# Kernel tuning notes

Hardware: AMD Instinct MI355X
Metric: run time of the kernel (lower is better)

The kernel has to match this reference:

```python
import jax, jax.numpy as jnp
import numpy as np

D = 2048      # hidden
H = 16        # heads
HD = 128      # head dim
E = 64        # experts
K = 8         # top-k
F = 1024      # expert intermediate
B, S = 1, 256
EPS = 1e-05
THETA = 10000.0
SCALE = 0.08838834764831845  # 1/sqrt(128)


def _rms(x, w):
    return x * jax.lax.rsqrt(jnp.mean(x * x, axis=-1, keepdims=True) + EPS) * w


def _rotate_half(x):
    h = x.shape[-1] // 2
    return jnp.concatenate([-x[..., h:], x[..., :h]], axis=-1)


def setup_inputs() -> dict:
    key = jax.random.key(0)
    ks = jax.random.split(key, 16)
    std = 0.02
    return {
        "x": jax.random.normal(ks[0], (B, S, D), jnp.float32),
        "ln1_w": jnp.ones((D,), jnp.float32),
        "q_w": jax.random.normal(ks[1], (D, D), jnp.float32) * std,
        "k_w": jax.random.normal(ks[2], (D, D), jnp.float32) * std,
        "v_w": jax.random.normal(ks[3], (D, D), jnp.float32) * std,
        "o_w": jax.random.normal(ks[4], (D, D), jnp.float32) * std,
        "qn_w": jnp.ones((D,), jnp.float32),
        "kn_w": jnp.ones((D,), jnp.float32),
        "ln2_w": jnp.ones((D,), jnp.float32),
        "router_w": jax.random.normal(ks[5], (E, D), jnp.float32) * std,
        "gate_w": jax.random.normal(ks[6], (E, F, D), jnp.float32) * std,
        "up_w": jax.random.normal(ks[7], (E, F, D), jnp.float32) * std,
        "down_w": jax.random.normal(ks[8], (E, D, F), jnp.float32) * std,
    }


def reference(x, ln1_w, q_w, k_w, v_w, o_w, qn_w, kn_w, ln2_w,
              router_w, gate_w, up_w, down_w):
    b, s, d = x.shape
    # ---- attention ----
    xn = _rms(x, ln1_w)
    q = _rms(jnp.einsum('bsd,od->bso', xn, q_w), qn_w)
    k = _rms(jnp.einsum('bsd,od->bso', xn, k_w), kn_w)
    v = jnp.einsum('bsd,od->bso', xn, v_w)
    q = q.reshape(b, s, H, HD).transpose(0, 2, 1, 3)  # [b,h,s,hd]
    k = k.reshape(b, s, H, HD).transpose(0, 2, 1, 3)
    v = v.reshape(b, s, H, HD).transpose(0, 2, 1, 3)
    # RoPE
    inv_freq = 1.0 / (THETA ** (jnp.arange(0, HD, 2, dtype=jnp.float32) / HD))
    ang = jnp.arange(s, dtype=jnp.float32)[:, None] * inv_freq[None, :]  # [s, hd/2]
    emb = jnp.concatenate([ang, ang], axis=-1)
    cos, sin = jnp.cos(emb).astype(x.dtype), jnp.sin(emb).astype(x.dtype)
    q = q * cos + _rotate_half(q) * sin
    k = k * cos + _rotate_half(k) * sin
    scores = jnp.einsum('bhqd,bhkd->bhqk', q, k) * SCALE
    causal = jnp.tril(jnp.ones((s, s), bool))
    scores = jnp.where(causal, scores, jnp.finfo(scores.dtype).min)
    attn = jax.nn.softmax(scores, axis=-1)
    ctx = jnp.einsum('bhqk,bhkd->bhqd', attn, v)
    ctx = ctx.transpose(0, 2, 1, 3).reshape(b, s, d)
    h = x + jnp.einsum('bsd,od->bso', ctx, o_w)
    # ---- MoE ----
    hn = _rms(h, ln2_w)
    logits = jnp.einsum('bsd,ed->bse', hn, router_w)
    probs = jax.nn.softmax(logits.astype(jnp.float32), axis=-1)
    vals, idx = jax.lax.top_k(probs, K)  # [b,s,K]
    # dense combine weights [b,s,E]; OLMoE does not renormalize top-k probs
    combine = jnp.sum(jax.nn.one_hot(idx, E, dtype=jnp.float32) * vals[..., None], axis=-2)
    combine = combine.reshape(-1, E).astype(x.dtype)  # [T,E]
    xf = hn.reshape(-1, d)                            # [T,D]
    g = jnp.einsum('td,efd->etf', xf, gate_w)         # [E,T,F]
    u = jnp.einsum('td,efd->etf', xf, up_w)
    mid = jax.nn.silu(g) * u
    eo = jnp.einsum('etf,edf->etd', mid, down_w)      # [E,T,D]
    y = jnp.einsum('te,etd->td', combine, eo).reshape(b, s, d)
    return h + y
```

## Files before the change

### kernel.cpp

```cpp
#include <hip/hip_runtime.h>
#include <math.h>

#define DHID 2048
#define TOK 256
#define NHEAD 16
#define HDIM 128
#define NEXP 64
#define KSEL 8
#define FFD 1024
#define RMSEPS 1e-5f
#define ATTNSCALE 0.08838834764831845f

typedef short bf16x8 __attribute__((ext_vector_type(8)));
typedef float f32x4 __attribute__((ext_vector_type(4)));
typedef float f4 __attribute__((ext_vector_type(4)));

__device__ __forceinline__ unsigned short f2bf(float f){
  union { float f; unsigned int u; } c; c.f = f;
  unsigned int u = c.u + 0x7fffu + ((c.u>>16)&1u);
  return (unsigned short)(u>>16);
}
__device__ __forceinline__ unsigned int pk2(float a, float b){
  return (unsigned int)f2bf(a) | ((unsigned int)f2bf(b)<<16);
}
__device__ __forceinline__ bf16x8 as_bf8(uint4 u){
  union { uint4 u; bf16x8 v; } c; c.u = u; return c.v;
}

#define WAITV(N) { asm volatile("s_waitcnt vmcnt(" #N ")" ::: "memory"); __builtin_amdgcn_sched_barrier(0); }
#define WAITL0   { asm volatile("s_waitcnt lgkmcnt(0)" ::: "memory"); __builtin_amdgcn_sched_barrier(0); }
#define SB       __builtin_amdgcn_sched_barrier(0);

__global__ __launch_bounds__(256) void rms_kernel(const float* __restrict__ x,
    const float* __restrict__ w, unsigned short* __restrict__ obf,
    float* __restrict__ of32)
{
  int row = blockIdx.x, tid = threadIdx.x;
  const float* xr = x + (size_t)row*DHID;
  float4 a = *(const float4*)(xr + tid*8);
  float4 b = *(const float4*)(xr + tid*8 + 4);
  float ss = a.x*a.x+a.y*a.y+a.z*a.z+a.w*a.w + b.x*b.x+b.y*b.y+b.z*b.z+b.w*b.w;
  #pragma unroll
  for(int o=32;o>0;o>>=1) ss += __shfl_down(ss,o);
  __shared__ float red[4];
  if((tid&63)==0) red[tid>>6]=ss;
  __syncthreads();
  float r = rsqrtf((red[0]+red[1]+red[2]+red[3])*(1.0f/DHID) + RMSEPS);
  float v[8] = {a.x,a.y,a.z,a.w,b.x,b.y,b.z,b.w};
  unsigned short ob[8];
  #pragma unroll
  for(int j=0;j<8;j++){
    float val = v[j]*r*w[tid*8+j];
    ob[j]=f2bf(val);
    if(of32) of32[(size_t)row*DHID + tid*8 + j] = val;
  }
  uint4 o4;
  o4.x = (unsigned int)ob[0] | ((unsigned int)ob[1]<<16);
  o4.y = (unsigned int)ob[2] | ((unsigned int)ob[3]<<16);
  o4.z = (unsigned int)ob[4] | ((unsigned int)ob[5]<<16);
  o4.w = (unsigned int)ob[6] | ((unsigned int)ob[7]<<16);
  *(uint4*)(obf + (size_t)row*DHID + tid*8) = o4;
}

__global__ void rope_table_kernel(float* __restrict__ cs, float* __restrict__ sn){
  int i = blockIdx.x*256 + threadIdx.x;
  int s = i>>6, j = i&63;
  float invf = powf(10000.0f, -(float)j*(1.0f/64.0f));
  float ang = (float)s * invf;
  cs[i] = cosf(ang); sn[i] = sinf(ang);
}

__global__ __launch_bounds__(256) void gemm_qkv_kernel(
    const unsigned short* __restrict__ A,
    const float* __restrict__ qw, const float* __restrict__ kw, const float* __restrict__ vw,
    float* __restrict__ qo, float* __restrict__ ko, float* __restrict__ vo)
{
  int nt = blockIdx.x, mt = blockIdx.y;
  int which = nt>>5, nb = nt&31;
  const float* W = (which==0)? qw : (which==1)? kw : vw;
  float* OUT = (which==0)? qo : (which==1)? ko : vo;
  int n0 = nb*64, m0 = mt*64;
  __shared__ unsigned short As[64*64];
  __shared__ unsigned short Bs[64*64];
  int tid = threadIdx.x;
  int wid = tid>>6, lane = tid&63;
  int wm = wid>>1, wn = wid&1;
  int lr = lane&15, lg = lane>>4;
  int sr = tid>>2, sq = tid&3;
  f32x4 acc[2][2] = {};
  const unsigned short* Ap = A + (size_t)(m0+sr)*DHID + sq*16;
  const float* Bp = W + (size_t)(n0+sr)*DHID + sq*16;
  for(int k0=0;k0<DHID;k0+=64){
    uint4 a0 = *(const uint4*)(Ap + k0);
    uint4 a1 = *(const uint4*)(Ap + k0 + 8);
    float4 b0 = *(const float4*)(Bp + k0);
    float4 b1 = *(const float4*)(Bp + k0 + 4);
    float4 b2 = *(const float4*)(Bp + k0 + 8);
    float4 b3 = *(const float4*)(Bp + k0 + 12);
    int x7 = sr&7;
    *(uint4*)&As[sr*64 + (((sq*2)  ^ x7)*8)] = a0;
    *(uint4*)&As[sr*64 + (((sq*2+1)^ x7)*8)] = a1;
    uint4 p0 = make_uint4(pk2(b0.x,b0.y),pk2(b0.z,b0.w),pk2(b1.x,b1.y),pk2(b1.z,b1.w));
    uint4 p1 = make_uint4(pk2(b2.x,b2.y),pk2(b2.z,b2.w),pk2(b3.x,b3.y),pk2(b3.z,b3.w));
    *(uint4*)&Bs[sr*64 + (((sq*2)  ^ x7)*8)] = p0;
    *(uint4*)&Bs[sr*64 + (((sq*2+1)^ x7)*8)] = p1;
    __syncthreads();
    #pragma unroll
    for(int ki=0;ki<2;ki++){
      bf16x8 af[2], bfr[2];
      #pragma unroll
      for(int mi=0;mi<2;mi++){
        int r = wm*32 + mi*16 + lr;
        af[mi] = *(const bf16x8*)&As[r*64 + (((ki*4+lg)^(r&7))*8)];
      }
      #pragma unroll
      for(int ni=0;ni<2;ni++){
        int r = wn*32 + ni*16 + lr;
        bfr[ni] = *(const bf16x8*)&Bs[r*64 + (((ki*4+lg)^(r&7))*8)];
      }
      #pragma unroll
      for(int mi=0;mi<2;mi++)
        #pragma unroll
        for(int ni=0;ni<2;ni++)
          acc[mi][ni] = __builtin_amdgcn_mfma_f32_16x16x32_bf16(af[mi], bfr[ni], acc[mi][ni], 0,0,0);
    }
    __syncthreads();
  }
  #pragma unroll
  for(int mi=0;mi<2;mi++){
    #pragma unroll
    for(int ni=0;ni<2;ni++){
      int col = n0 + wn*32 + ni*16 + lr;
      int rowb = m0 + wm*32 + mi*16 + lg*4;
      #pragma unroll
      for(int rg=0;rg<4;rg++)
        OUT[(size_t)(rowb+rg)*DHID + col] = acc[mi][ni][rg];
    }
  }
}

__global__ __launch_bounds__(256) void gemm_o_kernel(const float* __restrict__ A,
  const float* __restrict__ W, const float* __restrict__ X,
  float* __restrict__ H, float* __restrict__ O)
{
  int nb = blockIdx.x, mt = blockIdx.y;
  int n0 = nb*64, m0 = mt*64;
  __shared__ unsigned short As[64*64];
  __shared__ unsigned short Bs[64*64];
  int tid = threadIdx.x;
  int wid = tid>>6, lane = tid&63;
  int wm = wid>>1, wn = wid&1;
  int lr = lane&15, lg = lane>>4;
  int sr = tid>>2, sq = tid&3;
  f32x4 acc[2][2] = {};
  const float* Ap = A + (size_t)(m0+sr)*DHID + sq*16;
  const float* Bp = W + (size_t)(n0+sr)*DHID + sq*16;
  for(int k0=0;k0<DHID;k0+=64){
    float4 a0=*(const float4*)(Ap+k0),   a1=*(const float4*)(Ap+k0+4);
    float4 a2=*(const float4*)(Ap+k0+8), a3=*(const float4*)(Ap+k0+12);
    float4 b0=*(const float4*)(Bp+k0),   b1=*(const float4*)(Bp+k0+4);
    float4 b2=*(const float4*)(Bp+k0+8), b3=*(const float4*)(Bp+k0+12);
    int x7 = sr&7;
    uint4 pa0 = make_uint4(pk2(a0.x,a0.y),pk2(a0.z,a0.w),pk2(a1.x,a1.y),pk2(a1.z,a1.w));
    uint4 pa1 = make_uint4(pk2(a2.x,a2.y),pk2(a2.z,a2.w),pk2(a3.x,a3.y),pk2(a3.z,a3.w));
    uint4 pb0 = make_uint4(pk2(b0.x,b0.y),pk2(b0.z,b0.w),pk2(b1.x,b1.y),pk2(b1.z,b1.w));
    uint4 pb1 = make_uint4(pk2(b2.x,b2.y),pk2(b2.z,b2.w),pk2(b3.x,b3.y),pk2(b3.z,b3.w));
    *(uint4*)&As[sr*64 + (((sq*2)  ^ x7)*8)] = pa0;
    *(uint4*)&As[sr*64 + (((sq*2+1)^ x7)*8)] = pa1;
    *(uint4*)&Bs[sr*64 + (((sq*2)  ^ x7)*8)] = pb0;
    *(uint4*)&Bs[sr*64 + (((sq*2+1)^ x7)*8)] = pb1;
    __syncthreads();
    #pragma unroll
    for(int ki=0;ki<2;ki++){
      bf16x8 af[2], bfr[2];
      #pragma unroll
      for(int mi=0;mi<2;mi++){
        int r = wm*32 + mi*16 + lr;
        af[mi] = *(const bf16x8*)&As[r*64 + (((ki*4+lg)^(r&7))*8)];
      }
      #pragma unroll
      for(int ni=0;ni<2;ni++){
        int r = wn*32 + ni*16 + lr;
        bfr[ni] = *(const bf16x8*)&Bs[r*64 + (((ki*4+lg)^(r&7))*8)];
      }
      #pragma unroll
      for(int mi=0;mi<2;mi++)
        #pragma unroll
        for(int ni=0;ni<2;ni++)
          acc[mi][ni] = __builtin_amdgcn_mfma_f32_16x16x32_bf16(af[mi], bfr[ni], acc[mi][ni], 0,0,0);
    }
    __syncthreads();
  }
  #pragma unroll
  for(int mi=0;mi<2;mi++){
    #pragma unroll
    for(int ni=0;ni<2;ni++){
      int col = n0 + wn*32 + ni*16 + lr;
      int rowb = m0 + wm*32 + mi*16 + lg*4;
      #pragma unroll
      for(int rg=0;rg<4;rg++){
        size_t idx = (size_t)(rowb+rg)*DHID + col;
        float v = acc[mi][ni][rg] + X[idx];
        H[idx] = v; O[idx] = v;
      }
    }
  }
}

__global__ __launch_bounds__(256) void qknorm_rope_kernel(const float* __restrict__ in,
   const float* __restrict__ w, const float* __restrict__ cs, const float* __restrict__ sn,
   float* __restrict__ out)
{
  int t = blockIdx.x, tid = threadIdx.x;
  __shared__ float xs[DHID];
  const float* xr = in + (size_t)t*DHID;
  float4 a = *(const float4*)(xr + tid*8);
  float4 b = *(const float4*)(xr + tid*8 + 4);
  *(float4*)&xs[tid*8] = a; *(float4*)&xs[tid*8+4] = b;
  float ss = a.x*a.x+a.y*a.y+a.z*a.z+a.w*a.w + b.x*b.x+b.y*b.y+b.z*b.z+b.w*b.w;
  #pragma unroll
  for(int o=32;o>0;o>>=1) ss += __shfl_down(ss,o);
  __shared__ float red[4];
  if((tid&63)==0) red[tid>>6]=ss;
  __syncthreads();
  float r = rsqrtf((red[0]+red[1]+red[2]+red[3])*(1.0f/DHID) + RMSEPS);
  int hh = tid>>4, jb = (tid&15)*4;
  #pragma unroll
  for(int p=0;p<4;p++){
    int j = jb+p;
    int i0 = hh*HDIM + j, i1 = i0+64;
    float va = xs[i0]*r*w[i0];
    float vb = xs[i1]*r*w[i1];
    float c = cs[t*64+j], s = sn[t*64+j];
    out[((size_t)(hh*TOK + t))*HDIM + j]    = va*c - vb*s;
    out[((size_t)(hh*TOK + t))*HDIM + j+64] = vb*c + va*s;
  }
}

__global__ __launch_bounds__(256) void attn_kernel(const float* __restrict__ qh,
  const float* __restrict__ kh, const float* __restrict__ vf, float* __restrict__ ctx)
{
  int head = blockIdx.x>>4, qt = blockIdx.x&15;
  __shared__ float qs[16][132];
  __shared__ float sc[16][260];
  __shared__ float red[16][16];
  __shared__ float rmx[16], rsm[16];
  int tid = threadIdx.x;
  {
    int r = tid>>4, c = (tid&15)*8;
    const float* src = qh + ((size_t)(head*TOK + qt*16 + r))*HDIM + c;
    *(float4*)&qs[r][c]   = *(const float4*)(src);
    *(float4*)&qs[r][c+4] = *(const float4*)(src+4);
  }
  __syncthreads();
  int qi = tid&15, kk = tid>>4;
  int qg = qt*16 + qi;
  for(int k=kk; k<=qg; k+=16){
    const float* kp = kh + ((size_t)(head*TOK + k))*HDIM;
    float d = 0.f;
    #pragma unroll 8
    for(int c=0;c<128;c+=4){
      float4 kv = *(const float4*)(kp + c);
      float4 qv = *(const float4*)&qs[qi][c];
      d += qv.x*kv.x + qv.y*kv.y + qv.z*kv.z + qv.w*kv.w;
    }
    sc[qi][k] = d*ATTNSCALE;
  }
  float m = -1e30f;
  for(int k=kk;k<=qg;k+=16) m = fmaxf(m, sc[qi][k]);
  red[qi][kk] = m;
  __syncthreads();
  if(kk==0){
    float mm=-1e30f;
    #pragma unroll
    for(int j=0;j<16;j++) mm = fmaxf(mm, red[qi][j]);
    rmx[qi]=mm;
  }
  __syncthreads();
  float mm = rmx[qi];
  float s = 0.f;
  for(int k=kk;k<=qg;k+=16){ float pp = expf(sc[qi][k]-mm); sc[qi][k]=pp; s+=pp; }
  red[qi][kk]=s;
  __syncthreads();
  if(kk==0){
    float t_=0.f;
    #pragma unroll
    for(int j=0;j<16;j++) t_ += red[qi][j];
    rsm[qi]=t_;
  }
  __syncthreads();
  int dg = kk;
  float acc[8]={0,0,0,0,0,0,0,0};
  const float* vp = vf + head*HDIM + dg*8;
  for(int k=0;k<=qg;k++){
    float p = sc[qi][k];
    float4 v0 = *(const float4*)(vp + (size_t)k*DHID);
    float4 v1 = *(const float4*)(vp + (size_t)k*DHID + 4);
    acc[0]+=p*v0.x; acc[1]+=p*v0.y; acc[2]+=p*v0.z; acc[3]+=p*v0.w;
    acc[4]+=p*v1.x; acc[5]+=p*v1.y; acc[6]+=p*v1.z; acc[7]+=p*v1.w;
  }
  float inv = 1.0f/rsm[qi];
  float* op = ctx + ((size_t)(qt*16+qi))*DHID + head*HDIM + dg*8;
  *(float4*)(op)   = make_float4(acc[0]*inv, acc[1]*inv, acc[2]*inv, acc[3]*inv);
  *(float4*)(op+4) = make_float4(acc[4]*inv, acc[5]*inv, acc[6]*inv, acc[7]*inv);
}

__global__ __launch_bounds__(256) void router_kernel(const float* __restrict__ hn,
    const float* __restrict__ rw, int* __restrict__ counts, int* __restrict__ toklist,
    float* __restrict__ wlist)
{
  int t = blockIdx.x, tid = threadIdx.x;
  __shared__ float xs[DHID];
  __shared__ float part[NEXP*4];
  __shared__ float probs[NEXP];
  *(float4*)&xs[tid*8]   = *(const float4*)(hn + (size_t)t*DHID + tid*8);
  *(float4*)&xs[tid*8+4] = *(const float4*)(hn + (size_t)t*DHID + tid*8+4);
  __syncthreads();
  int e = tid&63, c = tid>>6;
  const float* w = rw + (size_t)e*DHID + c*512;
  const float* xc = xs + c*512;
  float d = 0.f;
  for(int i=0;i<512;i+=4){
    float4 wv = *(const float4*)(w+i);
    d += xc[i]*wv.x + xc[i+1]*wv.y + xc[i+2]*wv.z + xc[i+3]*wv.w;
  }
  part[c*64 + e] = d;
  __syncthreads();
  if(tid<64){
    float logit = part[tid] + part[64+tid] + part[128+tid] + part[192+tid];
    float m = logit;
    #pragma unroll
    for(int o=32;o>0;o>>=1) m = fmaxf(m, __shfl_xor(m,o));
    float p = expf(logit - m);
    float s = p;
    #pragma unroll
    for(int o=32;o>0;o>>=1) s += __shfl_xor(s,o);
    probs[tid] = p/s;
  }
  __syncthreads();
  if(tid==0){
    unsigned long long used = 0ull;
    for(int r=0;r<KSEL;r++){
      float best = -1.f; int bi = 0;
      for(int j=0;j<NEXP;j++){
        if(!((used>>j)&1ull) && probs[j]>best){ best=probs[j]; bi=j; }
      }
      used |= (1ull<<bi);
      int slot = atomicAdd(&counts[bi],1);
      toklist[bi*TOK+slot] = t;
      wlist[bi*TOK+slot] = best;
    }
  }
}

__global__ __launch_bounds__(256,2) void moe_gateup_kernel(const unsigned short* __restrict__ hnb,
  const float* __restrict__ gw, const float* __restrict__ uw,
  const int* __restrict__ counts,
  const int* __restrict__ toklist, const float* __restrict__ wlist,
  unsigned short* __restrict__ mid)
{
  int fb = blockIdx.x, e = blockIdx.y, mc = blockIdx.z;
  int cnt = counts[e];
  if(mc*32 >= cnt) return;
  int tid = threadIdx.x;
  __shared__ int sbase;
  if(tid<64){
    int c = counts[tid];
    int v = c;
    #pragma unroll
    for(int o=1;o<64;o<<=1){ int n=__shfl_up(v,o); if(tid>=o) v+=n; }
    if(tid==e) sbase = v - c;
  }
  __shared__ unsigned short Gs[64*256];
  __shared__ unsigned short Us[64*256];
  int w = tid>>6, lane = tid&63;
  int wm = w>>1, wn = w&1, lr = lane&15, lg = lane>>4;

  int r0 = w*16;
  const float* Gp = gw + ((size_t)e*FFD + fb*64 + r0)*DHID + lane*4;
  const float* Up = uw + ((size_t)e*FFD + fb*64 + r0)*DHID + lane*4;
  int aslot = mc*32 + wm*16 + lr;
  int acl = (aslot<cnt)? aslot : (cnt-1);
  const unsigned short* Ap = hnb + (size_t)toklist[e*TOK+acl]*DHID + lg*8;
  __syncthreads();
  int base = sbase;

  f32x4 ag[2]={}, au[2]={};
  f4 P[8], Q[8];
  uint4 av[8];

  int wu = lane>>1, wh = (lane&1)*4;

  #define ISSUE(BK,SRC,s,jb) { \
    _Pragma("unroll") \
    for(int j=0;j<8;j++) BK[j] = __builtin_nontemporal_load((const f4*)(SRC + (size_t)((jb)+j)*DHID + (s)*256)); }
  #define WRITE(BK,DST,jb) { \
    _Pragma("unroll") \
    for(int j=0;j<8;j++){ \
      int r = r0 + (jb) + j; \
      int p = (wu & ~15) | ((wu&15) ^ (r&15)); \
      uint2 val; val.x = pk2(BK[j][0],BK[j][1]); val.y = pk2(BK[j][2],BK[j][3]); \
      *(uint2*)&DST[r*256 + p*8 + wh] = val; } }
  #define ISSUE_A(s) { \
    _Pragma("unroll") \
    for(int kf=0;kf<8;kf++) av[kf] = *(const uint4*)(Ap + (s)*256 + kf*32); }
  #define COMPUTE() { \
    _Pragma("unroll") \
    for(int kf=0;kf<8;kf++){ \
      bf16x8 af = as_bf8(av[kf]); \
      _Pragma("unroll") \
      for(int ni=0;ni<2;ni++){ \
        int R = wn*32 + ni*16 + lr; \
        int v = kf*4 + lg; \
        int vp = (v & ~15) | ((v&15) ^ (R&15)); \
        int ho = R*256 + vp*8; \
        bf16x8 gfr = *(const bf16x8*)&Gs[ho]; \
        bf16x8 ufr = *(const bf16x8*)&Us[ho]; \
        ag[ni] = __builtin_amdgcn_mfma_f32_16x16x32_bf16(af, gfr, ag[ni], 0,0,0); \
        au[ni] = __builtin_amdgcn_mfma_f32_16x16x32_bf16(af, ufr, au[ni], 0,0,0); \
      } \
    } }

  const int NS = DHID/256;
  ISSUE(P, Gp, 0, 0)
  ISSUE(Q, Gp, 0, 8)
  for(int s=0;s<NS;s++){
    WAITV(8)
    WRITE(P, Gs, 0)
    ISSUE(P, Up, s, 0)
    WAITV(8)
    WRITE(Q, Gs, 8)
    ISSUE(Q, Up, s, 8)
    WAITV(8)
    WRITE(P, Us, 0)
    ISSUE_A(s)
    WAITV(8)
    WRITE(Q, Us, 8)
    if(s+1<NS){ ISSUE(P, Gp, s+1, 0) }
    WAITL0
    __builtin_amdgcn_s_barrier(); SB
    if(s+1<NS){ WAITV(8) } else { WAITV(0) }
    COMPUTE()
    if(s+1<NS){ ISSUE(Q, Gp, s+1, 8) }
    __builtin_amdgcn_s_barrier(); SB
  }
  #undef ISSUE
  #undef WRITE
  #undef ISSUE_A
  #undef COMPUTE

  #pragma unroll
  for(int ni=0;ni<2;ni++){
    int f = fb*64 + wn*32 + ni*16 + lr;
    #pragma unroll
    for(int rg=0;rg<4;rg++){
      int sl = wm*16 + lg*4 + rg;
      int slot = mc*32 + sl;
      if(slot < cnt){
        float cw = wlist[e*TOK + slot];
        float g = ag[ni][rg], u = au[ni][rg];
        float mval = g/(1.0f+expf(-g))*u*cw;
        mid[((size_t)(base+slot))*FFD + f] = f2bf(mval);
      }
    }
  }
}

__global__ __launch_bounds__(256,3) void moe_down_kernel(const unsigned short* __restrict__ mid,
  const float* __restrict__ dwn, const int* __restrict__ counts,
  const int* __restrict__ toklist, float* __restrict__ out)
{
  int nb=blockIdx.x, e=blockIdx.y, mc=blockIdx.z;
  int cnt=counts[e];
  if(mc*32>=cnt) return;
  int tid=threadIdx.x;
  __shared__ int sbase;
  if(tid<64){
    int c = counts[tid];
    int v = c;
    #pragma unroll
    for(int o=1;o<64;o<<=1){ int n=__shfl_up(v,o); if(tid>=o) v+=n; }
    if(tid==e) sbase = v - c;
  }
  __shared__ unsigned short Ds[64*256];
  int w=tid>>6, lane=tid&63;
  int wm=w>>1, wn=w&1, lr=lane&15, lg=lane>>4;
  int r0 = w*16;
  const float* Dp = dwn + ((size_t)e*DHID + nb*64 + r0)*FFD + lane*4;
  __syncthreads();
  int base = sbase;
  int slot0 = mc*32 + wm*16 + lr;
  int sla = (slot0<cnt)? slot0 : (cnt-1);
  const unsigned short* Ap = mid + (size_t)(base+sla)*FFD + lg*8;

  f32x4 acc[2]={};
  f4 P[8], Q[8];
  uint4 av[8];
  int wu = lane>>1, wh = (lane&1)*4;

  #define ISSUE(BK,s,jb) { \
    _Pragma("unroll") \
    for(int j=0;j<8;j++) BK[j] = __builtin_nontemporal_load((const f4*)(Dp + (size_t)((jb)+j)*FFD + (s)*256)); }
  #define WRITE(BK,jb) { \
    _Pragma("unroll") \
    for(int j=0;j<8;j++){ \
      int r = r0 + (jb) + j; \
      int p = (wu & ~15) | ((wu&15) ^ (r&15)); \
      uint2 val; val.x = pk2(BK[j][0],BK[j][1]); val.y = pk2(BK[j][2],BK[j][3]); \
      *(uint2*)&Ds[r*256 + p*8 + wh] = val; } }
  #define ISSUE_A(s) { \
    _Pragma("unroll") \
    for(int kf=0;kf<8;kf++) av[kf] = *(const uint4*)(Ap + (s)*256 + kf*32); }
  #define COMPUTE() { \
    _Pragma("unroll") \
    for(int kf=0;kf<8;kf++){ \
      bf16x8 af = as_bf8(av[kf]); \
      _Pragma("unroll") \
      for(int ni=0;ni<2;ni++){ \
        int R = wn*32 + ni*16 + lr; \
        int v = kf*4 + lg; \
        int vp = (v & ~15) | ((v&15) ^ (R&15)); \
        bf16x8 dfr = *(const bf16x8*)&Ds[R*256 + vp*8]; \
        acc[ni] = __builtin_amdgcn_mfma_f32_16x16x32_bf16(af, dfr, acc[ni], 0,0,0); \
      } \
    } }

  const int NS = FFD/256;
  ISSUE(P, 0, 0)
  ISSUE(Q, 0, 8)
  for(int s=0;s<NS;s++){
    WAITV(8)
    WRITE(P, 0)
    ISSUE_A(s)
    WAITV(8)
    WRITE(Q, 8)
    if(s+1<NS){ ISSUE(P, s+1, 0) }
    WAITL0
    __builtin_amdgcn_s_barrier(); SB
    if(s+1<NS){ WAITV(8) } else { WAITV(0) }
    COMPUTE()
    if(s+1<NS){ ISSUE(Q, s+1, 8) }
    __builtin_amdgcn_s_barrier(); SB
  }
  #undef ISSUE
  #undef WRITE
  #undef ISSUE_A
  #undef COMPUTE

  #pragma unroll
  for(int ni=0;ni<2;ni++){
    int d = nb*64 + wn*32 + ni*16 + lr;
    #pragma unroll
    for(int rg=0;rg<4;rg++){
      int sl=wm*16+lg*4+rg, slot=mc*32+sl;
      if(slot<cnt){
        int tok = toklist[e*TOK + slot];
        atomicAdd(out + (size_t)tok*DHID + d, acc[ni][rg]);
      }
    }
  }
}

extern "C" void kernel_launch(void* const* d_in, const int* in_sizes, int n_in,
                              void* d_out, int out_size, void* d_ws, size_t ws_size,
                              hipStream_t stream)
{
  (void)in_sizes; (void)n_in; (void)out_size; (void)ws_size;
  const float* x    = (const float*)d_in[0];
  const float* ln1w = (const float*)d_in[1];
  const float* qw   = (const float*)d_in[2];
  const float* kw   = (const float*)d_in[3];
  const float* vw   = (const float*)d_in[4];
  const float* ow   = (const float*)d_in[5];
  const float* qnw  = (const float*)d_in[6];
  const float* knw  = (const float*)d_in[7];
  const float* ln2w = (const float*)d_in[8];
  const float* rw   = (const float*)d_in[9];
  const float* gw   = (const float*)d_in[10];
  const float* uw   = (const float*)d_in[11];
  const float* dwn  = (const float*)d_in[12];
  float* out = (float*)d_out;

  char* p = (char*)d_ws;
  auto alloc = [&](size_t bytes)->void*{ void* r = (void*)p; p += (bytes + 255) & ~(size_t)255; return r; };
  unsigned short* xnb = (unsigned short*)alloc((size_t)TOK*DHID*2);
  float* qf   = (float*)alloc((size_t)TOK*DHID*4);
  float* kf   = (float*)alloc((size_t)TOK*DHID*4);
  float* vf   = (float*)alloc((size_t)TOK*DHID*4);
  float* qh   = (float*)alloc((size_t)TOK*DHID*4);
  float* kh   = (float*)alloc((size_t)TOK*DHID*4);
  float* ctx  = (float*)alloc((size_t)TOK*DHID*4);
  float* hbuf = (float*)alloc((size_t)TOK*DHID*4);
  float* hnf  = (float*)alloc((size_t)TOK*DHID*4);
  unsigned short* hnb = (unsigned short*)alloc((size_t)TOK*DHID*2);
  float* csb  = (float*)alloc((size_t)TOK*64*4);
  float* snb  = (float*)alloc((size_t)TOK*64*4);
  int* counts = (int*)alloc(NEXP*4);
  int* toklist= (int*)alloc((size_t)NEXP*TOK*4);
  float* wlist= (float*)alloc((size_t)NEXP*TOK*4);
  unsigned short* mid = (unsigned short*)alloc((size_t)TOK*KSEL*FFD*2);

  rope_table_kernel<<<64,256,0,stream>>>(csb,snb);
  rms_kernel<<<TOK,256,0,stream>>>(x, ln1w, xnb, nullptr);
  gemm_qkv_kernel<<<dim3(96,4),256,0,stream>>>(xnb,qw,kw,vw,qf,kf,vf);
  qknorm_rope_kernel<<<TOK,256,0,stream>>>(qf,qnw,csb,snb,qh);
  qknorm_rope_kernel<<<TOK,256,0,stream>>>(kf,knw,csb,snb,kh);
  attn_kernel<<<256,256,0,stream>>>(qh,kh,vf,ctx);
  gemm_o_kernel<<<dim3(32,4),256,0,stream>>>(ctx,ow,x,hbuf,out);
  rms_kernel<<<TOK,256,0,stream>>>(hbuf, ln2w, hnb, hnf);
  hipMemsetAsync(counts,0,NEXP*4,stream);
  router_kernel<<<TOK,256,0,stream>>>(hnf,rw,counts,toklist,wlist);
  moe_gateup_kernel<<<dim3(16,NEXP,8),256,0,stream>>>(hnb,gw,uw,counts,toklist,wlist,mid);
  moe_down_kernel<<<dim3(32,NEXP,8),256,0,stream>>>(mid,dwn,counts,toklist,out);
}
```

Measured before the change: 600.4 us.

## Enlarge MoE token tile to 128 so each expert weight tile is loaded once

Each MoE gate/up and down block now covers up to 128 routed tokens per expert instead of 32. Each wave handles four 16-token M sub-tiles, skipping empty ones, and the grid z-dimension drops from 8 to 2. Expert weight tiles are therefore converted to bf16 and staged in LDS once per 128 tokens rather than once per 32, cutting redundant fp32 weight traffic that dominates this memory-bound stage. The prefetch schedule is reordered, the A operand is now loaded inside compute, and the down kernel's launch bounds change, at the cost of more accumulator registers and fewer blocks.

New measurement: 584.6 us, median of 2. 2.6% less time.

```diff
diff --git a/kernel.cpp b/kernel.cpp
--- a/kernel.cpp
+++ b/kernel.cpp
@@ -361,7 +361,7 @@
 {
   int fb = blockIdx.x, e = blockIdx.y, mc = blockIdx.z;
   int cnt = counts[e];
-  if(mc*32 >= cnt) return;
+  if(mc*128 >= cnt) return;
   int tid = threadIdx.x;
   __shared__ int sbase;
   if(tid<64){
@@ -375,20 +375,23 @@
   __shared__ unsigned short Us[64*256];
   int w = tid>>6, lane = tid&63;
   int wm = w>>1, wn = w&1, lr = lane&15, lg = lane>>4;
+  int mbase = mc*128 + wm*64;
 
   int r0 = w*16;
   const float* Gp = gw + ((size_t)e*FFD + fb*64 + r0)*DHID + lane*4;
   const float* Up = uw + ((size_t)e*FFD + fb*64 + r0)*DHID + lane*4;
-  int aslot = mc*32 + wm*16 + lr;
-  int acl = (aslot<cnt)? aslot : (cnt-1);
-  const unsigned short* Ap = hnb + (size_t)toklist[e*TOK+acl]*DHID + lg*8;
+  const unsigned short* Ap[4];
+  #pragma unroll
+  for(int mi=0;mi<4;mi++){
+    int slot = mbase + mi*16 + lr;
+    int acl = (slot<cnt)? slot : (cnt-1);
+    Ap[mi] = hnb + (size_t)toklist[e*TOK+acl]*DHID + lg*8;
+  }
   __syncthreads();
   int base = sbase;
 
-  f32x4 ag[2]={}, au[2]={};
+  f32x4 ag[4][2]={}, au[4][2]={};
   f4 P[8], Q[8];
-  uint4 av[8];
-
   int wu = lane>>1, wh = (lane&1)*4;
 
   #define ISSUE(BK,SRC,s,jb) { \
@@ -401,23 +404,28 @@
       int p = (wu & ~15) | ((wu&15) ^ (r&15)); \
       uint2 val; val.x = pk2(BK[j][0],BK[j][1]); val.y = pk2(BK[j][2],BK[j][3]); \
       *(uint2*)&DST[r*256 + p*8 + wh] = val; } }
-  #define ISSUE_A(s) { \
+  #define COMPUTE(s) { \
     _Pragma("unroll") \
-    for(int kf=0;kf<8;kf++) av[kf] = *(const uint4*)(Ap + (s)*256 + kf*32); }
-  #define COMPUTE() { \
-    _Pragma("unroll") \
-    for(int kf=0;kf<8;kf++){ \
-      bf16x8 af = as_bf8(av[kf]); \
-      _Pragma("unroll") \
-      for(int ni=0;ni<2;ni++){ \
-        int R = wn*32 + ni*16 + lr; \
-        int v = kf*4 + lg; \
-        int vp = (v & ~15) | ((v&15) ^ (R&15)); \
-        int ho = R*256 + vp*8; \
-        bf16x8 gfr = *(const bf16x8*)&Gs[ho]; \
-        bf16x8 ufr = *(const bf16x8*)&Us[ho]; \
-        ag[ni] = __builtin_amdgcn_mfma_f32_16x16x32_bf16(af, gfr, ag[ni], 0,0,0); \
-        au[ni] = __builtin_amdgcn_mfma_f32_16x16x32_bf16(af, ufr, au[ni], 0,0,0); \
+    for(int mi=0;mi<4;mi++){ \
+      if(mbase + mi*16 < cnt){ \
+        uint4 av[8]; \
+        _Pragma("unroll") \
+        for(int kf=0;kf<8;kf++) av[kf] = *(const uint4*)(Ap[mi] + (size_t)(s)*256 + kf*32); \
+        _Pragma("unroll") \
+        for(int kf=0;kf<8;kf++){ \
+          bf16x8 af = as_bf8(av[kf]); \
+          _Pragma("unroll") \
+          for(int ni=0;ni<2;ni++){ \
+            int R = wn*32 + ni*16 + lr; \
+            int v = kf*4 + lg; \
+            int vp = (v & ~15) | ((v&15) ^ (R&15)); \
+            int ho = R*256 + vp*8; \
+            bf16x8 gfr = *(const bf16x8*)&Gs[ho]; \
+            bf16x8 ufr = *(const bf16x8*)&Us[ho]; \
+            ag[mi][ni] = __builtin_amdgcn_mfma_f32_16x16x32_bf16(af, gfr, ag[mi][ni], 0,0,0); \
+            au[mi][ni] = __builtin_amdgcn_mfma_f32_16x16x32_bf16(af, ufr, au[mi][ni], 0,0,0); \
+          } \
+        } \
       } \
     } }
 
@@ -433,46 +441,45 @@
     ISSUE(Q, Up, s, 8)
     WAITV(8)
     WRITE(P, Us, 0)
-    ISSUE_A(s)
-    WAITV(8)
+    if(s+1<NS){ ISSUE(P, Gp, s+1, 0) }
+    if(s+1<NS){ WAITV(8) } else { WAITV(0) }
     WRITE(Q, Us, 8)
-    if(s+1<NS){ ISSUE(P, Gp, s+1, 0) }
+    if(s+1<NS){ ISSUE(Q, Gp, s+1, 8) }
     WAITL0
     __builtin_amdgcn_s_barrier(); SB
-    if(s+1<NS){ WAITV(8) } else { WAITV(0) }
-    COMPUTE()
-    if(s+1<NS){ ISSUE(Q, Gp, s+1, 8) }
+    COMPUTE(s)
     __builtin_amdgcn_s_barrier(); SB
   }
   #undef ISSUE
   #undef WRITE
-  #undef ISSUE_A
   #undef COMPUTE
 
   #pragma unroll
-  for(int ni=0;ni<2;ni++){
-    int f = fb*64 + wn*32 + ni*16 + lr;
-    #pragma unroll
-    for(int rg=0;rg<4;rg++){
-      int sl = wm*16 + lg*4 + rg;
-      int slot = mc*32 + sl;
-      if(slot < cnt){
-        float cw = wlist[e*TOK + slot];
-        float g = ag[ni][rg], u = au[ni][rg];
-        float mval = g/(1.0f+expf(-g))*u*cw;
-        mid[((size_t)(base+slot))*FFD + f] = f2bf(mval);
-      }
-    }
-  }
-}
-
-__global__ __launch_bounds__(256,3) void moe_down_kernel(const unsigned short* __restrict__ mid,
+  for(int mi=0;mi<4;mi++){
+    #pragma unroll
+    for(int ni=0;ni<2;ni++){
+      int f = fb*64 + wn*32 + ni*16 + lr;
+      #pragma unroll
+      for(int rg=0;rg<4;rg++){
+        int slot = mbase + mi*16 + lg*4 + rg;
+        if(slot < cnt){
+          float cw = wlist[e*TOK + slot];
+          float g = ag[mi][ni][rg], u = au[mi][ni][rg];
+          float mval = g/(1.0f+expf(-g))*u*cw;
+          mid[((size_t)(base+slot))*FFD + f] = f2bf(mval);
+        }
+      }
+    }
+  }
+}
+
+__global__ __launch_bounds__(256,4) void moe_down_kernel(const unsigned short* __restrict__ mid,
   const float* __restrict__ dwn, const int* __restrict__ counts,
   const int* __restrict__ toklist, float* __restrict__ out)
 {
   int nb=blockIdx.x, e=blockIdx.y, mc=blockIdx.z;
   int cnt=counts[e];
-  if(mc*32>=cnt) return;
+  if(mc*128>=cnt) return;
   int tid=threadIdx.x;
   __shared__ int sbase;
   if(tid<64){
@@ -485,17 +492,21 @@
   __shared__ unsigned short Ds[64*256];
   int w=tid>>6, lane=tid&63;
   int wm=w>>1, wn=w&1, lr=lane&15, lg=lane>>4;
+  int mbase = mc*128 + wm*64;
   int r0 = w*16;
   const float* Dp = dwn + ((size_t)e*DHID + nb*64 + r0)*FFD + lane*4;
   __syncthreads();
   int base = sbase;
-  int slot0 = mc*32 + wm*16 + lr;
-  int sla = (slot0<cnt)? slot0 : (cnt-1);
-  const unsigned short* Ap = mid + (size_t)(base+sla)*FFD + lg*8;
-
-  f32x4 acc[2]={};
+  const unsigned short* Ap[4];
+  #pragma unroll
+  for(int mi=0;mi<4;mi++){
+    int slot = mbase + mi*16 + lr;
+    int acl = (slot<cnt)? slot : (cnt-1);
+    Ap[mi] = mid + (size_t)(base+acl)*FFD + lg*8;
+  }
+
+  f32x4 acc[4][2]={};
   f4 P[8], Q[8];
-  uint4 av[8];
   int wu = lane>>1, wh = (lane&1)*4;
 
   #define ISSUE(BK,s,jb) { \
@@ -508,20 +519,25 @@
       int p = (wu & ~15) | ((wu&15) ^ (r&15)); \
       uint2 val; val.x = pk2(BK[j][0],BK[j][1]); val.y = pk2(BK[j][2],BK[j][3]); \
       *(uint2*)&Ds[r*256 + p*8 + wh] = val; } }
-  #define ISSUE_A(s) { \
+  #define COMPUTE(s) { \
     _Pragma("unroll") \
-    for(int kf=0;kf<8;kf++) av[kf] = *(const uint4*)(Ap + (s)*256 + kf*32); }
-  #define COMPUTE() { \
-    _Pragma("unroll") \
-    for(int kf=0;kf<8;kf++){ \
-      bf16x8 af = as_bf8(av[kf]); \
-      _Pragma("unroll") \
-      for(int ni=0;ni<2;ni++){ \
-        int R = wn*32 + ni*16 + lr; \
-        int v = kf*4 + lg; \
-        int vp = (v & ~15) | ((v&15) ^ (R&15)); \
-        bf16x8 dfr = *(const bf16x8*)&Ds[R*256 + vp*8]; \
-        acc[ni] = __builtin_amdgcn_mfma_f32_16x16x32_bf16(af, dfr, acc[ni], 0,0,0); \
+    for(int mi=0;mi<4;mi++){ \
+      if(mbase + mi*16 < cnt){ \
+        uint4 av[8]; \
+        _Pragma("unroll") \
+        for(int kf=0;kf<8;kf++) av[kf] = *(const uint4*)(Ap[mi] + (size_t)(s)*256 + kf*32); \
+        _Pragma("unroll") \
+        for(int kf=0;kf<8;kf++){ \
+          bf16x8 af = as_bf8(av[kf]); \
+          _Pragma("unroll") \
+          for(int ni=0;ni<2;ni++){ \
+            int R = wn*32 + ni*16 + lr; \
+            int v = kf*4 + lg; \
+            int vp = (v & ~15) | ((v&15) ^ (R&15)); \
+            bf16x8 dfr = *(const bf16x8*)&Ds[R*256 + vp*8]; \
+            acc[mi][ni] = __builtin_amdgcn_mfma_f32_16x16x32_bf16(af, dfr, acc[mi][ni], 0,0,0); \
+          } \
+        } \
       } \
     } }
 
@@ -531,31 +547,31 @@
   for(int s=0;s<NS;s++){
     WAITV(8)
     WRITE(P, 0)
-    ISSUE_A(s)
-    WAITV(8)
+    if(s+1<NS){ ISSUE(P, s+1, 0) }
+    if(s+1<NS){ WAITV(8) } else { WAITV(0) }
     WRITE(Q, 8)
-    if(s+1<NS){ ISSUE(P, s+1, 0) }
+    if(s+1<NS){ ISSUE(Q, s+1, 8) }
     WAITL0
     __builtin_amdgcn_s_barrier(); SB
-    if(s+1<NS){ WAITV(8) } else { WAITV(0) }
-    COMPUTE()
-    if(s+1<NS){ ISSUE(Q, s+1, 8) }
+    COMPUTE(s)
     __builtin_amdgcn_s_barrier(); SB
   }
   #undef ISSUE
   #undef WRITE
-  #undef ISSUE_A
   #undef COMPUTE
 
   #pragma unroll
-  for(int ni=0;ni<2;ni++){
-    int d = nb*64 + wn*32 + ni*16 + lr;
-    #pragma unroll
-    for(int rg=0;rg<4;rg++){
-      int sl=wm*16+lg*4+rg, slot=mc*32+sl;
-      if(slot<cnt){
-        int tok = toklist[e*TOK + slot];
-        atomicAdd(out + (size_t)tok*DHID + d, acc[ni][rg]);
+  for(int mi=0;mi<4;mi++){
+    #pragma unroll
+    for(int ni=0;ni<2;ni++){
+      int d = nb*64 + wn*32 + ni*16 + lr;
+      #pragma unroll
+      for(int rg=0;rg<4;rg++){
+        int slot = mbase + mi*16 + lg*4 + rg;
+        if(slot<cnt){
+          int tok = toklist[e*TOK + slot];
+          atomicAdd(out + (size_t)tok*DHID + d, acc[mi][ni][rg]);
+        }
       }
     }
   }
@@ -610,6 +626,6 @@
   rms_kernel<<<TOK,256,0,stream>>>(hbuf, ln2w, hnb, hnf);
   hipMemsetAsync(counts,0,NEXP*4,stream);
   router_kernel<<<TOK,256,0,stream>>>(hnf,rw,counts,toklist,wlist);
-  moe_gateup_kernel<<<dim3(16,NEXP,8),256,0,stream>>>(hnb,gw,uw,counts,toklist,wlist,mid);
-  moe_down_kernel<<<dim3(32,NEXP,8),256,0,stream>>>(mid,dwn,counts,toklist,out);
-}
+  moe_gateup_kernel<<<dim3(16,NEXP,2),256,0,stream>>>(hnb,gw,uw,counts,toklist,wlist,mid);
+  moe_down_kernel<<<dim3(32,NEXP,2),256,0,stream>>>(mid,dwn,counts,toklist,out);
+}
```
